# Performance work log

Hardware: AMD Instinct MI355X
Metric: run time of the kernel (lower is better)

The kernel has to match this reference:

```python
import jax, jax.numpy as jnp
import numpy as np

MAX_SHIFT_BANDS = 2.0


def setup_inputs() -> dict:
    key = jax.random.key(0)
    k1, k2 = jax.random.split(key)
    B, Bh, H, W = 4, 128, 256, 256
    x = jax.random.normal(k1, (B, Bh, H, W), dtype=jnp.float32)
    wavelength_shift = jax.random.normal(k2, (B, Bh, W), dtype=jnp.float32)
    return {"x": x, "wavelength_shift": wavelength_shift}


def reference(x, wavelength_shift):
    # Faithful to torch grid_sample(mode='bilinear', padding_mode='border',
    # align_corners=False) applied along the spectral (band) axis only.
    B, Bh, H, W = x.shape
    dt = x.dtype

    shift = jnp.clip(wavelength_shift, -MAX_SHIFT_BANDS, MAX_SHIFT_BANDS)
    shift = shift[:, :, None, :]                         # [B,Bh,1,W]
    band = jnp.arange(Bh, dtype=dt)[None, :, None, None]  # [1,Bh,1,1]
    shifted = jnp.clip(band + shift, 0.0, Bh - 1)        # [B,Bh,1,W]

    # grid_sample align_corners=False unnormalization:
    # grid g = shifted/(Bh-1)*2 - 1 ; iy = ((g+1)*Bh - 1)/2 = shifted*Bh/(Bh-1) - 0.5
    iy = shifted * (Bh / (Bh - 1)) - 0.5                 # [B,Bh,1,W]
    i0f = jnp.floor(iy)
    w = iy - i0f                                          # lerp weight, [B,Bh,1,W]
    i0 = i0f.astype(jnp.int32)                            # may be -1 at low edge
    i0c = jnp.clip(i0, 0, Bh - 1)                         # border padding
    i1c = jnp.clip(i0 + 1, 0, Bh - 1)

    # broadcast gather indices over H rows
    i0c = jnp.broadcast_to(i0c, (B, Bh, H, W))
    i1c = jnp.broadcast_to(i1c, (B, Bh, H, W))

    x0 = jnp.take_along_axis(x, i0c, axis=1)              # [B,Bh,H,W]
    x1 = jnp.take_along_axis(x, i1c, axis=1)
    return x0 * (1.0 - w) + x1 * w
```

## Files before the change

kernel.cpp:

```cpp
#include <hip/hip_runtime.h>


#define BH_ 128
#define H_  256
#define W_  256
#define TB   32
#define NLDS (TB + 6)
#define RPT  16

__global__ __launch_bounds__(512) void smile_kernel(
    const float* __restrict__ x,
    const float* __restrict__ ws,
    float* __restrict__ out)
{
    __shared__ float tile[NLDS][W_];

    const int t = threadIdx.x;
    int bid = blockIdx.x;
    const int tileI = bid & 3;
    bid >>= 2;
    const int h = bid & (H_ - 1);
    const int b = bid >> 8;
    const int bh0 = tileI * TB;

    const int wave = t >> 6;
    const int lane = t & 63;
    const int w  = t & (W_ - 1);
    const int hr = t >> 8;

    const float* __restrict__ xsrc = x + (size_t)b * (BH_ * H_ * W_) + h * W_;
    for (int i = wave; i < NLDS; i += 8) {
        const int band = min(max(bh0 - 3 + i, 0), BH_ - 1);
        const float* gp = xsrc + (size_t)band * (H_ * W_) + lane * 4;
        __builtin_amdgcn_global_load_lds(
            (const __attribute__((address_space(1))) void*)gp,
            (__attribute__((address_space(3))) void*)&tile[i][0],
            16, 0, 0);
    }

    const int bhbase = bh0 + hr * RPT;
    const float* __restrict__ wsb = ws + (size_t)(b * BH_ + bhbase) * W_ + w;
    float s[RPT];
#pragma unroll
    for (int r = 0; r < RPT; ++r)
        s[r] = wsb[r * W_];

    __syncthreads();

    const float scale = (float)(128.0 / 127.0);
    float* __restrict__ outb =
        out + (((size_t)b * BH_ + bhbase) * H_ + h) * W_ + w;

#pragma unroll
    for (int r = 0; r < RPT; ++r) {
        const int bh = bhbase + r;
        float sc      = fminf(fmaxf(s[r], -2.0f), 2.0f);
        float shifted = fminf(fmaxf((float)bh + sc, 0.0f), (float)(BH_ - 1));
        float iy      = fmaf(shifted, scale, -0.5f);
        float i0f     = floorf(iy);
        float frac    = iy - i0f;
        int   i0      = (int)i0f;
        int   r0      = min(max(i0, 0), BH_ - 1) - bh0 + 3;
        int   r1      = min(i0 + 1, BH_ - 1) - bh0 + 3;
        float x0 = tile[r0][w];
        float x1 = tile[r1][w];
        outb[(size_t)r * (H_ * W_)] = fmaf(frac, x1 - x0, x0);
    }
}

extern "C" void kernel_launch(void* const* d_in, const int* in_sizes, int n_in,
                              void* d_out, int out_size, void* d_ws, size_t ws_size,
                              hipStream_t stream) {
    const float* x  = (const float*)d_in[0];
    const float* ws = (const float*)d_in[1];
    float* out = (float*)d_out;

    const int grid = 4 * H_ * (BH_ / TB);
    smile_kernel<<<grid, 512, 0, stream>>>(x, ws, out);
}
```

Baseline: 48.92 us.

## Double-buffer band tiles across four stages per block with async LDS loads

Each block now processes all four 32-band tiles for one (b,h) row instead of one tile, with a ping-pong LDS buffer. The next tile's global-to-LDS loads and shift loads are issued before computing the current tile, and partial vmcnt waits let loads overlap compute. The grid shrinks fourfold and LDS use roughly doubles, which reduces occupancy and parallelism. The hand-tuned vmcnt counts must match the instruction ordering the compiler emits.

```diff
diff --git a/kernel.cpp b/kernel.cpp
--- a/kernel.cpp
+++ b/kernel.cpp
@@ -1,71 +1,102 @@
 #include <hip/hip_runtime.h>
 
 
-#define BH_ 128
-#define H_  256
-#define W_  256
-#define TB   32
-#define NLDS (TB + 6)
-#define RPT  16
+#define BH_   128
+#define H_    256
+#define W_    256
+#define TB    32
+#define NROWS 38
+#define RPT   16
 
 __global__ __launch_bounds__(512) void smile_kernel(
     const float* __restrict__ x,
     const float* __restrict__ ws,
     float* __restrict__ out)
 {
-    __shared__ float tile[NLDS][W_];
+    __shared__ float lds[(2 * NROWS + 1) * W_];
 
-    const int t = threadIdx.x;
-    int bid = blockIdx.x;
-    const int tileI = bid & 3;
-    bid >>= 2;
-    const int h = bid & (H_ - 1);
-    const int b = bid >> 8;
-    const int bh0 = tileI * TB;
+    const int t   = threadIdx.x;
+    const int bid = blockIdx.x;
+    const int h   = bid & (H_ - 1);
+    const int b   = bid >> 8;
 
     const int wave = t >> 6;
     const int lane = t & 63;
-    const int w  = t & (W_ - 1);
-    const int hr = t >> 8;
+    const int w    = t & (W_ - 1);
+    const int hr   = t >> 8;
 
     const float* __restrict__ xsrc = x + (size_t)b * (BH_ * H_ * W_) + h * W_;
-    for (int i = wave; i < NLDS; i += 8) {
-        const int band = min(max(bh0 - 3 + i, 0), BH_ - 1);
-        const float* gp = xsrc + (size_t)band * (H_ * W_) + lane * 4;
-        __builtin_amdgcn_global_load_lds(
-            (const __attribute__((address_space(1))) void*)gp,
-            (__attribute__((address_space(3))) void*)&tile[i][0],
-            16, 0, 0);
-    }
+    const float* __restrict__ wsb  = ws + (size_t)b * BH_ * W_ + w;
+    float* __restrict__ outb = out + ((size_t)b * BH_ * H_ + h) * W_ + w;
 
-    const int bhbase = bh0 + hr * RPT;
-    const float* __restrict__ wsb = ws + (size_t)(b * BH_ + bhbase) * W_ + w;
-    float s[RPT];
+    auto STAGE = [&](int k, int base) {
+        const int bh0 = k * TB;
 #pragma unroll
-    for (int r = 0; r < RPT; ++r)
-        s[r] = wsb[r * W_];
+        for (int j = 0; j < 5; ++j) {
+            const int i    = wave + j * 8;
+            const bool rl  = (i < NROWS);
+            const int band = min(max(bh0 - 3 + (rl ? i : 0), 0), BH_ - 1);
+            const float* gp = xsrc + (size_t)band * (H_ * W_) + lane * 4;
+            float* lp = &lds[(rl ? (base + i) : (2 * NROWS)) * W_];
+            __builtin_amdgcn_global_load_lds(
+                (const __attribute__((address_space(1))) void*)gp,
+                (__attribute__((address_space(3))) void*)lp, 16, 0, 0);
+        }
+    };
+    auto WSLOAD = [&](int k, float* s) {
+#pragma unroll
+        for (int r = 0; r < RPT; ++r)
+            s[r] = wsb[(k * TB + hr * RPT + r) * W_];
+    };
+    auto COMPUTE = [&](int k, int base, const float* s) {
+        const int bh0 = k * TB;
+        const float scale = (float)(128.0 / 127.0);
+#pragma unroll
+        for (int r = 0; r < RPT; ++r) {
+            const int bh  = bh0 + hr * RPT + r;
+            float sc      = fminf(fmaxf(s[r], -2.0f), 2.0f);
+            float shifted = fminf(fmaxf((float)bh + sc, 0.0f), 127.0f);
+            float iy      = fmaf(shifted, scale, -0.5f);
+            float i0f     = floorf(iy);
+            float frac    = iy - i0f;
+            int   i0      = (int)i0f;
+            int   r0      = min(max(i0, 0), BH_ - 1) - bh0 + 3;
+            int   r1      = min(i0 + 1, BH_ - 1) - bh0 + 3;
+            float x0 = lds[(base + r0) * W_ + w];
+            float x1 = lds[(base + r1) * W_ + w];
+            outb[(size_t)bh * (H_ * W_)] = fmaf(frac, x1 - x0, x0);
+        }
+    };
 
-    __syncthreads();
+    float s0[RPT], s1[RPT];
 
-    const float scale = (float)(128.0 / 127.0);
-    float* __restrict__ outb =
-        out + (((size_t)b * BH_ + bhbase) * H_ + h) * W_ + w;
+    STAGE(0, 0);
+    WSLOAD(0, s0);
 
-#pragma unroll
-    for (int r = 0; r < RPT; ++r) {
-        const int bh = bhbase + r;
-        float sc      = fminf(fmaxf(s[r], -2.0f), 2.0f);
-        float shifted = fminf(fmaxf((float)bh + sc, 0.0f), (float)(BH_ - 1));
-        float iy      = fmaf(shifted, scale, -0.5f);
-        float i0f     = floorf(iy);
-        float frac    = iy - i0f;
-        int   i0      = (int)i0f;
-        int   r0      = min(max(i0, 0), BH_ - 1) - bh0 + 3;
-        int   r1      = min(i0 + 1, BH_ - 1) - bh0 + 3;
-        float x0 = tile[r0][w];
-        float x1 = tile[r1][w];
-        outb[(size_t)r * (H_ * W_)] = fmaf(frac, x1 - x0, x0);
-    }
+    STAGE(1, NROWS);
+    WSLOAD(1, s1);
+    asm volatile("s_waitcnt vmcnt(21)" ::: "memory");
+    __builtin_amdgcn_s_barrier();
+    COMPUTE(0, 0, s0);
+    __builtin_amdgcn_s_barrier();
+
+    STAGE(2, 0);
+    WSLOAD(2, s0);
+    asm volatile("s_waitcnt vmcnt(21)" ::: "memory");
+    __builtin_amdgcn_s_barrier();
+    COMPUTE(1, NROWS, s1);
+    __builtin_amdgcn_s_barrier();
+
+    STAGE(3, NROWS);
+    WSLOAD(3, s1);
+    asm volatile("s_waitcnt vmcnt(21)" ::: "memory");
+    __builtin_amdgcn_s_barrier();
+    COMPUTE(2, 0, s0);
+    __builtin_amdgcn_s_barrier();
+
+    asm volatile("s_waitcnt vmcnt(0)" ::: "memory");
+    __builtin_amdgcn_s_barrier();
+    COMPUTE(3, NROWS, s1);
 }
 
 extern "C" void kernel_launch(void* const* d_in, const int* in_sizes, int n_in,
@@ -75,6 +106,6 @@
     const float* ws = (const float*)d_in[1];
     float* out = (float*)d_out;
 
-    const int grid = 4 * H_ * (BH_ / TB);
+    const int grid = 4 * H_;
     smile_kernel<<<grid, 512, 0, stream>>>(x, ws, out);
 }
```

Measured after the change: 50.13 us. 1.02x slower.
